# Performance work log

Hardware: AMD Instinct MI355X
Metric: run time of the kernel (lower is better)

Reference implementation:

```python
import jax, jax.numpy as jnp
import numpy as np

# --- model constants (reconstructed LIF + exponential-PSP semantics) ---
V_TH = 1.0        # spike threshold
V_DECAY = 0.9     # membrane leak per ms
PSP_DECAY = 0.8   # postsynaptic-potential filter decay
BETA = 5.0        # surrogate-gradient sharpness
D = 16            # spike_buffer depth (max synaptic delay)
H = W = 64
T = 200
N = H * W
N_DEL = 11        # number of delayed synapses


def setup_inputs() -> dict:
    key = jax.random.key(0)
    ks = jax.random.split(key, 5)
    stim = jax.random.uniform(ks[0], (H, W, T), dtype=jnp.float32) * 8.0
    scale = 1.0 / np.sqrt(N)
    W_sa_in = jax.random.normal(ks[1], (N, N), dtype=jnp.float32) * scale
    W_ra_in = jax.random.normal(ks[2], (N, N), dtype=jnp.float32) * scale
    W_del = jax.random.normal(ks[3], (N_DEL, N, N), dtype=jnp.float32) * scale
    delays = jax.random.randint(ks[4], (N_DEL, N), 0, D, dtype=jnp.int32)
    return {"stim": stim, "W_sa_in": W_sa_in, "W_ra_in": W_ra_in,
            "W_del": W_del, "delays": delays}


def _spike(v):
    """Hard threshold forward, sigmoid surrogate gradient (straight-through)."""
    hard = (v >= V_TH).astype(v.dtype)
    soft = jax.nn.sigmoid(BETA * (v - V_TH))
    return soft + jax.lax.stop_gradient(hard - soft)


def reference(stim, W_sa_in, W_ra_in, W_del, delays):
    n = stim.shape[0] * stim.shape[1]
    t_len = stim.shape[2]
    # stimulus preprocessing (feedforward):
    sa_stim = (stim - 3.0).reshape(n, t_len)                    # [N, T]
    d = jnp.abs(jnp.diff(stim, axis=2)) * 10.0                  # [H, W, T-1]
    d = d.at[:, :, :3].set(0.0)
    ra_stim = jnp.concatenate(
        [jnp.zeros(stim.shape[:2] + (1,), stim.dtype), d], axis=2
    ).reshape(n, t_len)                                         # [N, T]

    idx = jnp.arange(n)
    read_col = D - 1 - delays                                   # [11, N] constant gather columns

    def lif(v, buf, li, inp):
        vn = v[li] * V_DECAY + inp
        s = _spike(vn)
        vn = vn * (1.0 - s)                                     # reset on spike
        v = v.at[li].set(vn)
        buf = buf.at[li].set(
            jnp.concatenate([buf[li][:, 1:], s[:, None]], axis=1))  # roll, newest last
        return v, buf, s

    def syn(psp, k, buf_pre):
        dsp = buf_pre[idx, read_col[k]]                         # per-pre delayed spikes [N]
        p = psp[k] * PSP_DECAY + W_del[k] @ dsp
        return psp.at[k].set(p), p

    def step(carry, xs):
        v, buf, psp = carry
        sa_x, ra_x = xs
        # SA pathway (layers 0,1,2 <-> state rows 0,1,2)
        v, buf, s0 = lif(v, buf, 0, W_sa_in @ sa_x)
        psp, i1 = syn(psp, 0, buf[0])
        v, buf, s1 = lif(v, buf, 1, i1)
        psp, pn1 = syn(psp, 1, buf[0])
        psp, pn2 = syn(psp, 2, buf[1])
        v, buf, s2 = lif(v, buf, 2, 2.0 * pn1 - pn2)
        # RA pathway (state rows 3,4,5)
        v, buf, s3 = lif(v, buf, 3, W_ra_in @ ra_x)
        psp, j1 = syn(psp, 3, buf[3])
        v, buf, s4 = lif(v, buf, 4, j1)
        psp, qn1 = syn(psp, 4, buf[3])
        psp, qn2 = syn(psp, 5, buf[4])
        v, buf, s5 = lif(v, buf, 5, 2.0 * qn1 - qn2)
        # CN (state rows 6 = IN, 7 = PN)
        psp, cin_sa = syn(psp, 6, buf[2])
        psp, cin_ra = syn(psp, 8, buf[5])
        v, buf, s6 = lif(v, buf, 6, cin_sa + cin_ra)
        psp, cpn_sa = syn(psp, 7, buf[2])
        psp, cpn_ra = syn(psp, 9, buf[5])
        psp, inh = syn(psp, 10, buf[6])
        v, buf, s7 = lif(v, buf, 7, 2.0 * cpn_sa + 2.0 * cpn_ra - inh)
        return (v, buf, psp), jnp.stack([s0, s1, s2, s3, s4, s5, s6, s7])

    carry0 = (jnp.zeros((8, n), stim.dtype),
              jnp.zeros((8, n, D), stim.dtype),
              jnp.zeros((N_DEL, n), stim.dtype))
    xs = (sa_stim[:, 1:].T, ra_stim[:, 1:].T)                   # [T-1, N] each
    _, spikes = jax.lax.scan(step, carry0, xs)                  # [T-1, 8, N]
    return jnp.transpose(spikes, (1, 2, 0))                     # [8, N, T-1]
```

## Files before the change

### kernel.cpp

```cpp
#include <hip/hip_runtime.h>

#define NN   4096
#define TLEN 200
#define NT   199
#define NW   8
#define NTP  256
#define TN   ((size_t)NT * NN)
#define TN2  ((size_t)NN * NTP)

#define BM 128
#define BT 128
#define BK 32
#define BMP 132
#define BTP 132

typedef __attribute__((ext_vector_type(8))) short short8;
typedef __attribute__((ext_vector_type(16))) float f32x16;


__global__ __launch_bounds__(256, 2) void gsyn(const float* __restrict__ Wdel,
    const int* __restrict__ delays, const unsigned* __restrict__ Sb,
    float* __restrict__ u, int Slog, int kpack, int prepack, int slotpack) {
  const int z = blockIdx.y;
  const int ki = z >> Slog, s = z & ((1 << Slog) - 1);
  const int k = (kpack >> (4 * ki)) & 15;
  const int pre = (prepack >> (4 * ki)) & 15;
  const int slot = ((slotpack >> (6 * ki)) & 63) + s;
  const int NJ = NN >> Slog;
  const int jbase = s * NJ;
  const float* __restrict__ Wk = Wdel + (size_t)k * NN * NN;
  const unsigned* __restrict__ Sp = Sb + (size_t)pre * NW * NN;
  const int* __restrict__ dl = delays + (size_t)k * NN;
  float* __restrict__ uo = u + (size_t)slot * TN2;

  __shared__ __align__(16) unsigned char smem[3 * 8192 + 16384];
  #define XOFF 24576

  const int i0 = blockIdx.x * 128;
  const int tid = threadIdx.x;
  const int wave = tid >> 6, lane = tid & 63;
  const int m = lane & 31, hb = lane >> 5;
  const int wi = wave >> 1, wt = wave & 1;

  f32x16 acc[2][4];
  #pragma unroll
  for (int a = 0; a < 2; ++a)
    #pragma unroll
    for (int b = 0; b < 4; ++b) acc[a][b] = 0.0f;

  const int rb = tid >> 3, kc = tid & 7;
  const int kx = tid & 31, tg = tid >> 5;

  for (int j0 = 0; j0 < NJ; j0 += 32) {
    #pragma unroll
    for (int mm = 0; mm < 4; ++mm) {
      const int r = rb + 32 * mm;
      const float4 w4 = *(const float4*)&Wk[(size_t)(i0 + r) * NN + jbase + j0 + kc * 4];
      unsigned h[4], md[4], lo[4];
      const float wv[4] = {w4.x, w4.y, w4.z, w4.w};
      #pragma unroll
      for (int e = 0; e < 4; ++e) {
        const unsigned ub = __float_as_uint(wv[e]);
        h[e] = ub >> 16;
        const float r1 = wv[e] - __uint_as_float(ub & 0xFFFF0000u);
        const unsigned u1 = __float_as_uint(r1);
        md[e] = u1 >> 16;
        const float r2 = r1 - __uint_as_float(u1 & 0xFFFF0000u);
        lo[e] = __float_as_uint(r2) >> 16;
      }
      const unsigned base = (unsigned)((r * 64 + kc * 8) ^ ((r & 7) << 4));
      uint2 p0; p0.x = (h[1] << 16) | h[0];  p0.y = (h[3] << 16) | h[2];
      uint2 p1; p1.x = (md[1] << 16) | md[0]; p1.y = (md[3] << 16) | md[2];
      uint2 p2; p2.x = (lo[1] << 16) | lo[0]; p2.y = (lo[3] << 16) | lo[2];
      *(uint2*)(smem + base)          = p0;
      *(uint2*)(smem + 8192 + base)   = p1;
      *(uint2*)(smem + 16384 + base)  = p2;
    }
    {
      const int j = jbase + j0 + kx;
      const int d = dl[j];
      const int tsrc = tg * 32 - d;
      const int w0 = tsrc >> 5;
      const int sh = tsrc & 31;
      const unsigned blo = (w0 >= 0) ? Sp[(size_t)w0 * NN + j] : 0u;
      const unsigned bhi = (w0 + 1 < NW) ? Sp[(size_t)(w0 + 1) * NN + j] : 0u;
      const unsigned wnd = sh ? ((blo >> sh) | (bhi << (32 - sh))) : blo;
      #pragma unroll
      for (int b = 0; b < 32; ++b) {
        const unsigned short xv = ((wnd >> b) & 1u) ? (unsigned short)0x3F80 : (unsigned short)0;
        const int t = tg * 32 + b;
        *(unsigned short*)(smem + XOFF + ((t * 64 + kx * 2) ^ ((t & 7) << 4))) = xv;
      }
    }
    __syncthreads();
    #pragma unroll
    for (int h2 = 0; h2 < 2; ++h2) {
      const int cb = h2 * 32 + hb * 16;
      short8 bfr[4];
      #pragma unroll
      for (int b = 0; b < 4; ++b) {
        const int tr = wt * 128 + b * 32 + m;
        bfr[b] = *(const short8*)(smem + XOFF + ((tr * 64 + cb) ^ ((tr & 7) << 4)));
      }
      #pragma unroll
      for (int a = 0; a < 2; ++a) {
        const int ra = wi * 64 + a * 32 + m;
        const unsigned abase = (unsigned)((ra * 64 + cb) ^ ((ra & 7) << 4));
        const short8 a0 = *(const short8*)(smem + abase);
        const short8 a1 = *(const short8*)(smem + 8192 + abase);
        const short8 a2 = *(const short8*)(smem + 16384 + abase);
        #pragma unroll
        for (int b = 0; b < 4; ++b) {
          acc[a][b] = __builtin_amdgcn_mfma_f32_32x32x16_bf16(a0, bfr[b], acc[a][b], 0, 0, 0);
          acc[a][b] = __builtin_amdgcn_mfma_f32_32x32x16_bf16(a1, bfr[b], acc[a][b], 0, 0, 0);
          acc[a][b] = __builtin_amdgcn_mfma_f32_32x32x16_bf16(a2, bfr[b], acc[a][b], 0, 0, 0);
        }
      }
    }
    __syncthreads();
  }
  #pragma unroll
  for (int a = 0; a < 2; ++a)
    #pragma unroll
    for (int b = 0; b < 4; ++b) {
      const int tt2 = wt * 128 + b * 32 + m;
      #pragma unroll
      for (int r = 0; r < 16; ++r) {
        const int ii = i0 + wi * 64 + a * 32 + (r & 3) + 8 * (r >> 2) + 4 * hb;
        uo[(size_t)ii * NTP + tt2] = acc[a][b][r];
      }
    }
  #undef XOFF
}

__global__ __launch_bounds__(256, 2) void gstim(const float* __restrict__ Wsa,
    const float* __restrict__ Wra, const float* __restrict__ stim,
    float* __restrict__ u) {
  const int zi = blockIdx.z;
  const int mode = zi >> 2, s = zi & 3;
  const int slot = 64 + 4 * mode + s;
  const int NJ = NN >> 2;
  const int jbase = s * NJ;
  const float* __restrict__ W = mode ? Wra : Wsa;
  float* __restrict__ uo = u + (size_t)slot * TN2;

  __shared__ float Ws[BK][BMP];
  __shared__ float Xs[BK][BTP];
  const int i0 = blockIdx.x * BM;
  const int t0 = blockIdx.y * BT;
  const int tid = threadIdx.x;
  const int rg = tid >> 4, cg = tid & 15;
  float acc[8][8] = {};

  for (int k0 = 0; k0 < NJ; k0 += BK) {
    {
      const int kk4 = tid & 7, r = tid >> 3;
      const int sw = 4 * kk4;
      #pragma unroll
      for (int mq = 0; mq < 4; ++mq) {
        const int rr = r + 32 * mq;
        const float4 w = *(const float4*)&W[(size_t)(i0 + rr) * NN + jbase + k0 + 4 * kk4];
        const int pc = rr ^ sw;
        Ws[4 * kk4 + 0][pc] = w.x; Ws[4 * kk4 + 1][pc] = w.y;
        Ws[4 * kk4 + 2][pc] = w.z; Ws[4 * kk4 + 3][pc] = w.w;
      }
    }
    {
      const int kk = tid >> 3, sb8 = tid & 7;
      const int j = jbase + k0 + kk;
      #pragma unroll
      for (int q = 0; q < 4; ++q) {
        float4 xv;
        float* xp = (float*)&xv;
        #pragma unroll
        for (int e = 0; e < 4; ++e) {
          const int tt = t0 + 16 * sb8 + 4 * q + e;
          float x = 0.0f;
          if (tt < NT) {
            const int tc = tt + 1;
            if (mode == 0) {
              x = stim[(size_t)j * TLEN + tc] - 3.0f;
            } else {
              x = (tc >= 4)
                ? fabsf(stim[(size_t)j * TLEN + tc] - stim[(size_t)j * TLEN + tc - 1]) * 10.0f
                : 0.0f;
            }
          }
          xp[e] = x;
        }
        *(float4*)&Xs[kk][16 * sb8 + 4 * q] = xv;
      }
    }
    __syncthreads();
    #pragma unroll
    for (int kk = 0; kk < BK; ++kk) {
      const int wsw = 4 * (kk >> 2);
      const float4 ra = *(const float4*)&Ws[kk][(rg * 4) ^ wsw];
      const float4 rbv = *(const float4*)&Ws[kk][(64 + rg * 4) ^ wsw];
      const float4 ca = *(const float4*)&Xs[kk][cg * 4];
      const float4 cb = *(const float4*)&Xs[kk][64 + cg * 4];
      const float rv[8] = {ra.x, ra.y, ra.z, ra.w, rbv.x, rbv.y, rbv.z, rbv.w};
      const float cv[8] = {ca.x, ca.y, ca.z, ca.w, cb.x, cb.y, cb.z, cb.w};
      #pragma unroll
      for (int a = 0; a < 8; ++a)
        #pragma unroll
        for (int b = 0; b < 8; ++b) acc[a][b] += rv[a] * cv[b];
    }
    __syncthreads();
  }
  #pragma unroll
  for (int a = 0; a < 8; ++a) {
    const int ia = i0 + ((a < 4) ? (rg * 4 + a) : (64 + rg * 4 + (a - 4)));
    #pragma unroll
    for (int bh = 0; bh < 2; ++bh) {
      float4 o;
      o.x = acc[a][bh * 4 + 0]; o.y = acc[a][bh * 4 + 1];
      o.z = acc[a][bh * 4 + 2]; o.w = acc[a][bh * 4 + 3];
      *(float4*)&uo[(size_t)ia * NTP + t0 + bh * 64 + cg * 4] = o;
    }
  }
}

template<int S>
__device__ __forceinline__ float4 sumS4(const float* __restrict__ u, int slot, int tg, int j) {
  float4 r = {0.f, 0.f, 0.f, 0.f};
  #pragma unroll
  for (int q = 0; q < S; ++q) {
    const float4 a = *(const float4*)&u[(size_t)(slot + q) * TN2 + (size_t)j * NTP + tg];
    r.x += a.x; r.y += a.y; r.z += a.z; r.w += a.w;
  }
  return r;
}
__device__ __forceinline__ float fidx(const float4& v, int q) {
  return q == 0 ? v.x : q == 1 ? v.y : q == 2 ? v.z : v.w;
}

__device__ __forceinline__ void flush_bits(unsigned* sb, int j, int t, unsigned& bits) {
  if ((t & 31) == 31 || t == NT - 1) { sb[(size_t)(t >> 5) * NN + j] = bits; bits = 0; }
}

__global__ void scan_a(const float* __restrict__ u, unsigned* __restrict__ Sb) {
  const int j = blockIdx.x * 64 + threadIdx.x;
  const int base = 64 + 4 * blockIdx.y;
  unsigned* sb = Sb + (size_t)(blockIdx.y ? 3 : 0) * NW * NN;
  float v = 0.f; unsigned bits = 0;
  for (int tg = 0; tg < NT; tg += 4) {
    const float4 in4 = sumS4<4>(u, base, tg, j);
    #pragma unroll
    for (int q = 0; q < 4; ++q) {
      const int t = tg + q;
      if (t < NT) {
        float vn = v * 0.9f + fidx(in4, q);
        unsigned s = vn >= 1.0f;
        v = s ? 0.f : vn;
        bits |= s << (t & 31);
        flush_bits(sb, j, t, bits);
      }
    }
  }
}

__global__ void scan_b(const float* __restrict__ u, unsigned* __restrict__ Sb,
                       float* __restrict__ p1s, float* __restrict__ p4s) {
  const int j = blockIdx.x * 64 + threadIdx.x;
  const int sa = blockIdx.y;
  const int baseA = sa ? 8 : 0, baseB = sa ? 12 : 4;
  float* ps = sa ? p4s : p1s;
  unsigned* sb = Sb + (size_t)(sa ? 4 : 1) * NW * NN;
  float v = 0.f, pa = 0.f, pb = 0.f; unsigned bits = 0;
  for (int tg = 0; tg < NT; tg += 4) {
    const float4 A4 = sumS4<4>(u, baseA, tg, j);
    const float4 B4 = sumS4<4>(u, baseB, tg, j);
    #pragma unroll
    for (int q = 0; q < 4; ++q) {
      const int t = tg + q;
      if (t < NT) {
        pa = pa * 0.8f + fidx(A4, q);
        float vn = v * 0.9f + pa;
        unsigned s = vn >= 1.0f;
        v = s ? 0.f : vn;
        bits |= s << (t & 31);
        flush_bits(sb, j, t, bits);
        pb = pb * 0.8f + fidx(B4, q);
        ps[(size_t)t * NN + j] = 2.0f * pb;
      }
    }
  }
}

__global__ void scan_c(const float* __restrict__ u, unsigned* __restrict__ Sb,
                       const float* __restrict__ p1s, const float* __restrict__ p4s) {
  const int j = blockIdx.x * 64 + threadIdx.x;
  const int sa = blockIdx.y;
  const int base = sa ? 24 : 16;
  const float* ps = sa ? p4s : p1s;
  unsigned* sb = Sb + (size_t)(sa ? 5 : 2) * NW * NN;
  float v = 0.f, p = 0.f; unsigned bits = 0;
  for (int tg = 0; tg < NT; tg += 4) {
    const float4 A4 = sumS4<8>(u, base, tg, j);
    float P[4];
    #pragma unroll
    for (int q = 0; q < 4; ++q)
      P[q] = (tg + q < NT) ? ps[(size_t)(tg + q) * NN + j] : 0.0f;
    #pragma unroll
    for (int q = 0; q < 4; ++q) {
      const int t = tg + q;
      if (t < NT) {
        p = p * 0.8f + fidx(A4, q);
        float vn = v * 0.9f + (P[q] - p);
        unsigned s = vn >= 1.0f;
        v = s ? 0.f : vn;
        bits |= s << (t & 31);
        flush_bits(sb, j, t, bits);
      }
    }
  }
}

__global__ void scan_d(const float* __restrict__ u, unsigned* __restrict__ Sb,
                       float* __restrict__ p79s) {
  const int j = blockIdx.x * 64 + threadIdx.x;
  if (blockIdx.y == 0) {
    unsigned* sb = Sb + (size_t)6 * NW * NN;
    float v = 0.f, p6 = 0.f, p8 = 0.f; unsigned bits = 0;
    for (int tg = 0; tg < NT; tg += 4) {
      const float4 A4 = sumS4<4>(u, 32, tg, j);
      const float4 B4 = sumS4<4>(u, 40, tg, j);
      #pragma unroll
      for (int q = 0; q < 4; ++q) {
        const int t = tg + q;
        if (t < NT) {
          p6 = p6 * 0.8f + fidx(A4, q);
          p8 = p8 * 0.8f + fidx(B4, q);
          float vn = v * 0.9f + (p6 + p8);
          unsigned s = vn >= 1.0f;
          v = s ? 0.f : vn;
          bits |= s << (t & 31);
          flush_bits(sb, j, t, bits);
        }
      }
    }
  } else {
    float p7 = 0.f, p9 = 0.f;
    for (int tg = 0; tg < NT; tg += 4) {
      const float4 A4 = sumS4<4>(u, 36, tg, j);
      const float4 B4 = sumS4<4>(u, 44, tg, j);
      #pragma unroll
      for (int q = 0; q < 4; ++q) {
        const int t = tg + q;
        if (t < NT) {
          p7 = p7 * 0.8f + fidx(A4, q);
          p9 = p9 * 0.8f + fidx(B4, q);
          p79s[(size_t)t * NN + j] = 2.0f * p7 + 2.0f * p9;
        }
      }
    }
  }
}

__global__ void scan_e(const float* __restrict__ u, unsigned* __restrict__ Sb,
                       const float* __restrict__ p79s) {
  const int j = blockIdx.x * 64 + threadIdx.x;
  unsigned* sb = Sb + (size_t)7 * NW * NN;
  float v = 0.f, p = 0.f; unsigned bits = 0;
  for (int tg = 0; tg < NT; tg += 4) {
    const float4 A4 = sumS4<16>(u, 48, tg, j);
    float P[4];
    #pragma unroll
    for (int q = 0; q < 4; ++q)
      P[q] = (tg + q < NT) ? p79s[(size_t)(tg + q) * NN + j] : 0.0f;
    #pragma unroll
    for (int q = 0; q < 4; ++q) {
      const int t = tg + q;
      if (t < NT) {
        p = p * 0.8f + fidx(A4, q);
        float vn = v * 0.9f + (P[q] - p);
        unsigned s = vn >= 1.0f;
        v = s ? 0.f : vn;
        bits |= s << (t & 31);
        flush_bits(sb, j, t, bits);
      }
    }
  }
}

__global__ void expand_k(const unsigned* __restrict__ Sb, float* __restrict__ out) {
  const int j = blockIdx.x * 256 + threadIdx.x;
  const int w = blockIdx.y, li = blockIdx.z;
  unsigned bits = Sb[((size_t)li * NW + w) * NN + j];
  float* o = out + ((size_t)li * NN + j) * NT + w * 32;
  int nb = NT - w * 32; if (nb > 32) nb = 32;
  for (int b = 0; b < nb; ++b) o[b] = (float)((bits >> b) & 1u);
}

extern "C" void kernel_launch(void* const* d_in, const int* in_sizes, int n_in,
                              void* d_out, int out_size, void* d_ws, size_t ws_size,
                              hipStream_t stream) {
  const float* stim   = (const float*)d_in[0];
  const float* Wsa    = (const float*)d_in[1];
  const float* Wra    = (const float*)d_in[2];
  const float* Wdel   = (const float*)d_in[3];
  const int*   delays = (const int*)d_in[4];
  float* out = (float*)d_out;
  float* ws  = (float*)d_ws;

  float* u    = ws;
  float* p1s  = u + 72 * TN2;
  float* p4s  = p1s + TN;
  float* p79s = p4s + TN;
  unsigned* Sb = (unsigned*)(p79s + TN);
  size_t need = (72 * TN2 + 3 * TN + (size_t)8 * NW * NN) * 4;
  if (ws_size < need) return;

  hipMemsetAsync(Sb, 0, (size_t)8 * NW * NN * sizeof(unsigned), stream);

  const dim3 gmf(NN / 128, 16);
  gstim<<<dim3(NN / BM, 2, 8), 256, 0, stream>>>(Wsa, Wra, stim, u);
  scan_a<<<dim3(64, 2), 64, 0, stream>>>(u, Sb);

  gsyn<<<gmf, 256, 0, stream>>>(Wdel, delays, Sb, u, 2, 0x4310, 0x3300,
                                0 | (4 << 6) | (8 << 12) | (12 << 18));
  scan_b<<<dim3(64, 2), 64, 0, stream>>>(u, Sb, p1s, p4s);

  gsyn<<<gmf, 256, 0, stream>>>(Wdel, delays, Sb, u, 3, 0x52, 0x41, 16 | (24 << 6));
  scan_c<<<dim3(64, 2), 64, 0, stream>>>(u, Sb, p1s, p4s);

  gsyn<<<gmf, 256, 0, stream>>>(Wdel, delays, Sb, u, 2, 0x9876, 0x5522,
                                32 | (36 << 6) | (40 << 12) | (44 << 18));
  scan_d<<<dim3(64, 2), 64, 0, stream>>>(u, Sb, p79s);

  gsyn<<<gmf, 256, 0, stream>>>(Wdel, delays, Sb, u, 4, 10, 6, 48);
  scan_e<<<dim3(64, 1), 64, 0, stream>>>(u, Sb, p79s);

  expand_k<<<dim3(16, 7, 8), 256, 0, stream>>>(Sb, out);
}
```

Measured before the change: 803.8 us.

## Precompute delayed spike bf16 matrix in separate kernel, load B operand from global

Adds an xmat kernel that expands the delayed spike bitmasks into a dense bf16 [k][t][j] matrix in workspace once per stage. gsyn then loads its MFMA B fragments straight from global memory into registers instead of rebuilding them per tile with 32 scalar shared-memory stores per thread. This removes redundant per-block expansion, which every i-tile repeated, and shrinks shared memory. The cost is four extra launches and extra global traffic for the dense X matrix, read by every i-block.

```diff
diff --git a/kernel.cpp b/kernel.cpp
--- a/kernel.cpp
+++ b/kernel.cpp
@@ -18,23 +18,55 @@
 typedef __attribute__((ext_vector_type(16))) float f32x16;
 
 
+__global__ void xmat(const int* __restrict__ delays, const unsigned* __restrict__ Sb,
+                     unsigned short* __restrict__ Xg, int kpack, int prepack) {
+  const int ki = blockIdx.y;
+  const int k = (kpack >> (4 * ki)) & 15;
+  const int pre = (prepack >> (4 * ki)) & 15;
+  const int jb = blockIdx.x * 32;
+  __shared__ unsigned Xw[32][8];
+  const int tid = threadIdx.x;
+  {
+    const int jj = tid >> 3, tw = tid & 7;
+    const int j = jb + jj;
+    const int d = delays[(size_t)k * NN + j];
+    const int tsrc = tw * 32 - d;
+    const int w0 = tsrc >> 5, sh = tsrc & 31;
+    const unsigned lo = (w0 >= 0 && w0 < NW) ? Sb[(size_t)pre * NW * NN + (size_t)w0 * NN + j] : 0u;
+    const unsigned hi = (w0 + 1 >= 0 && w0 + 1 < NW) ? Sb[(size_t)pre * NW * NN + (size_t)(w0 + 1) * NN + j] : 0u;
+    Xw[jj][tw] = sh ? ((lo >> sh) | (hi << (32 - sh))) : lo;
+  }
+  __syncthreads();
+  {
+    const int t = tid;
+    const int tw = t >> 5, tb = t & 31;
+    unsigned out[16];
+    #pragma unroll
+    for (int q = 0; q < 16; ++q) {
+      const unsigned b0 = (Xw[2 * q][tw] >> tb) & 1u;
+      const unsigned b1 = (Xw[2 * q + 1][tw] >> tb) & 1u;
+      out[q] = (b0 ? 0x3F80u : 0u) | (b1 ? 0x3F800000u : 0u);
+    }
+    unsigned short* dst = Xg + ((size_t)k * NTP + t) * NN + jb;
+    #pragma unroll
+    for (int q = 0; q < 4; ++q) *(uint4*)(dst + 8 * q) = *(uint4*)&out[4 * q];
+  }
+}
+
 __global__ __launch_bounds__(256, 2) void gsyn(const float* __restrict__ Wdel,
-    const int* __restrict__ delays, const unsigned* __restrict__ Sb,
-    float* __restrict__ u, int Slog, int kpack, int prepack, int slotpack) {
+    const unsigned short* __restrict__ Xg, float* __restrict__ u,
+    int Slog, int kpack, int slotpack) {
   const int z = blockIdx.y;
   const int ki = z >> Slog, s = z & ((1 << Slog) - 1);
   const int k = (kpack >> (4 * ki)) & 15;
-  const int pre = (prepack >> (4 * ki)) & 15;
   const int slot = ((slotpack >> (6 * ki)) & 63) + s;
   const int NJ = NN >> Slog;
   const int jbase = s * NJ;
   const float* __restrict__ Wk = Wdel + (size_t)k * NN * NN;
-  const unsigned* __restrict__ Sp = Sb + (size_t)pre * NW * NN;
-  const int* __restrict__ dl = delays + (size_t)k * NN;
+  const unsigned short* __restrict__ Xk = Xg + (size_t)k * NTP * NN;
   float* __restrict__ uo = u + (size_t)slot * TN2;
 
-  __shared__ __align__(16) unsigned char smem[3 * 8192 + 16384];
-  #define XOFF 24576
+  __shared__ __align__(16) unsigned char smem[3 * 8192];
 
   const int i0 = blockIdx.x * 128;
   const int tid = threadIdx.x;
@@ -49,9 +81,16 @@
     for (int b = 0; b < 4; ++b) acc[a][b] = 0.0f;
 
   const int rb = tid >> 3, kc = tid & 7;
-  const int kx = tid & 31, tg = tid >> 5;
+  const unsigned short* __restrict__ xp0 = Xk + (size_t)(wt * 128 + m) * NN + jbase;
 
   for (int j0 = 0; j0 < NJ; j0 += 32) {
+    short8 xb[2][4];
+    #pragma unroll
+    for (int h2 = 0; h2 < 2; ++h2)
+      #pragma unroll
+      for (int b = 0; b < 4; ++b)
+        xb[h2][b] = *(const short8*)(xp0 + (size_t)(b * 32) * NN + j0 + h2 * 16 + hb * 8);
+
     #pragma unroll
     for (int mm = 0; mm < 4; ++mm) {
       const int r = rb + 32 * mm;
@@ -76,32 +115,10 @@
       *(uint2*)(smem + 8192 + base)   = p1;
       *(uint2*)(smem + 16384 + base)  = p2;
     }
-    {
-      const int j = jbase + j0 + kx;
-      const int d = dl[j];
-      const int tsrc = tg * 32 - d;
-      const int w0 = tsrc >> 5;
-      const int sh = tsrc & 31;
-      const unsigned blo = (w0 >= 0) ? Sp[(size_t)w0 * NN + j] : 0u;
-      const unsigned bhi = (w0 + 1 < NW) ? Sp[(size_t)(w0 + 1) * NN + j] : 0u;
-      const unsigned wnd = sh ? ((blo >> sh) | (bhi << (32 - sh))) : blo;
-      #pragma unroll
-      for (int b = 0; b < 32; ++b) {
-        const unsigned short xv = ((wnd >> b) & 1u) ? (unsigned short)0x3F80 : (unsigned short)0;
-        const int t = tg * 32 + b;
-        *(unsigned short*)(smem + XOFF + ((t * 64 + kx * 2) ^ ((t & 7) << 4))) = xv;
-      }
-    }
     __syncthreads();
     #pragma unroll
     for (int h2 = 0; h2 < 2; ++h2) {
       const int cb = h2 * 32 + hb * 16;
-      short8 bfr[4];
-      #pragma unroll
-      for (int b = 0; b < 4; ++b) {
-        const int tr = wt * 128 + b * 32 + m;
-        bfr[b] = *(const short8*)(smem + XOFF + ((tr * 64 + cb) ^ ((tr & 7) << 4)));
-      }
       #pragma unroll
       for (int a = 0; a < 2; ++a) {
         const int ra = wi * 64 + a * 32 + m;
@@ -111,9 +128,9 @@
         const short8 a2 = *(const short8*)(smem + 16384 + abase);
         #pragma unroll
         for (int b = 0; b < 4; ++b) {
-          acc[a][b] = __builtin_amdgcn_mfma_f32_32x32x16_bf16(a0, bfr[b], acc[a][b], 0, 0, 0);
-          acc[a][b] = __builtin_amdgcn_mfma_f32_32x32x16_bf16(a1, bfr[b], acc[a][b], 0, 0, 0);
-          acc[a][b] = __builtin_amdgcn_mfma_f32_32x32x16_bf16(a2, bfr[b], acc[a][b], 0, 0, 0);
+          acc[a][b] = __builtin_amdgcn_mfma_f32_32x32x16_bf16(a0, xb[h2][b], acc[a][b], 0, 0, 0);
+          acc[a][b] = __builtin_amdgcn_mfma_f32_32x32x16_bf16(a1, xb[h2][b], acc[a][b], 0, 0, 0);
+          acc[a][b] = __builtin_amdgcn_mfma_f32_32x32x16_bf16(a2, xb[h2][b], acc[a][b], 0, 0, 0);
         }
       }
     }
@@ -130,7 +147,6 @@
         uo[(size_t)ii * NTP + tt2] = acc[a][b][r];
       }
     }
-  #undef XOFF
 }
 
 __global__ __launch_bounds__(256, 2) void gstim(const float* __restrict__ Wsa,
@@ -409,7 +425,8 @@
   float* p4s  = p1s + TN;
   float* p79s = p4s + TN;
   unsigned* Sb = (unsigned*)(p79s + TN);
-  size_t need = (72 * TN2 + 3 * TN + (size_t)8 * NW * NN) * 4;
+  unsigned short* Xg = (unsigned short*)(Sb + (size_t)8 * NW * NN);
+  size_t need = (72 * TN2 + 3 * TN + (size_t)8 * NW * NN) * 4 + (size_t)11 * NTP * NN * 2;
   if (ws_size < need) return;
 
   hipMemsetAsync(Sb, 0, (size_t)8 * NW * NN * sizeof(unsigned), stream);
@@ -418,18 +435,22 @@
   gstim<<<dim3(NN / BM, 2, 8), 256, 0, stream>>>(Wsa, Wra, stim, u);
   scan_a<<<dim3(64, 2), 64, 0, stream>>>(u, Sb);
 
-  gsyn<<<gmf, 256, 0, stream>>>(Wdel, delays, Sb, u, 2, 0x4310, 0x3300,
+  xmat<<<dim3(NN / 32, 4), 256, 0, stream>>>(delays, Sb, Xg, 0x4310, 0x3300);
+  gsyn<<<gmf, 256, 0, stream>>>(Wdel, Xg, u, 2, 0x4310,
                                 0 | (4 << 6) | (8 << 12) | (12 << 18));
   scan_b<<<dim3(64, 2), 64, 0, stream>>>(u, Sb, p1s, p4s);
 
-  gsyn<<<gmf, 256, 0, stream>>>(Wdel, delays, Sb, u, 3, 0x52, 0x41, 16 | (24 << 6));
+  xmat<<<dim3(NN / 32, 2), 256, 0, stream>>>(delays, Sb, Xg, 0x52, 0x41);
+  gsyn<<<gmf, 256, 0, stream>>>(Wdel, Xg, u, 3, 0x52, 16 | (24 << 6));
   scan_c<<<dim3(64, 2), 64, 0, stream>>>(u, Sb, p1s, p4s);
 
-  gsyn<<<gmf, 256, 0, stream>>>(Wdel, delays, Sb, u, 2, 0x9876, 0x5522,
+  xmat<<<dim3(NN / 32, 4), 256, 0, stream>>>(delays, Sb, Xg, 0x9876, 0x5522);
+  gsyn<<<gmf, 256, 0, stream>>>(Wdel, Xg, u, 2, 0x9876,
                                 32 | (36 << 6) | (40 << 12) | (44 << 18));
   scan_d<<<dim3(64, 2), 64, 0, stream>>>(u, Sb, p79s);
 
-  gsyn<<<gmf, 256, 0, stream>>>(Wdel, delays, Sb, u, 4, 10, 6, 48);
+  xmat<<<dim3(NN / 32, 1), 256, 0, stream>>>(delays, Sb, Xg, 10, 6);
+  gsyn<<<gmf, 256, 0, stream>>>(Wdel, Xg, u, 4, 10, 48);
   scan_e<<<dim3(64, 1), 64, 0, stream>>>(u, Sb, p79s);
 
   expand_k<<<dim3(16, 7, 8), 256, 0, stream>>>(Sb, out);
```

After: 831.1 us. 3.4% more time.
